# Kernel tuning notes

Measured on AMD Instinct MI355X. Metric: run time of the kernel, lower is better.

Reference implementation:

```python
import jax, jax.numpy as jnp
import numpy as np

NUM_CLASSES = 172
IGNORE_INDEX = 255
DICE_WEIGHT = 0.5
EPS = 1e-7


def setup_inputs() -> dict:
    key = jax.random.key(0)
    k1, k2 = jax.random.split(key)
    pred = jax.random.normal(k1, (4, NUM_CLASSES, 256, 256), dtype=jnp.float32)
    target = jax.random.randint(k2, (4, 256, 256), 0, NUM_CLASSES, dtype=jnp.int32)
    return {"pred": pred, "target": target}


def reference(pred, target):
    # pred: [B, C, H, W] logits; target: [B, H, W] int labels (255 = ignore)
    C = NUM_CLASSES
    logp = jax.nn.log_softmax(pred, axis=1)  # [B, C, H, W]

    # ---- cross entropy with ignore_index (mean over valid pixels) ----
    valid = target != IGNORE_INDEX  # [B, H, W]
    safe_tgt = jnp.where(valid, target, 0)
    nll = -jnp.take_along_axis(logp, safe_tgt[:, None].astype(jnp.int32), axis=1)[:, 0]  # [B, H, W]
    n_valid = jnp.sum(valid)
    ce = jnp.sum(jnp.where(valid, nll, 0.0)) / jnp.maximum(n_valid, 1).astype(pred.dtype)

    # ---- dice loss: vectorized over classes (replaces per-class python loop) ----
    p = jnp.exp(logp)  # softmax probs [B, C, H, W]
    # intersection[c] = sum over pixels with target==c of p[:, c] at those pixels
    gathered = jnp.take_along_axis(p, safe_tgt[:, None].astype(jnp.int32), axis=1)[:, 0]  # [B, H, W]
    seg_ids = target.ravel().astype(jnp.int32)  # ignore pixels land in bucket 255, discarded
    inter = jax.ops.segment_sum(gathered.ravel(), seg_ids, num_segments=256)[:C]  # [C]
    counts = jax.ops.segment_sum(jnp.ones_like(gathered.ravel()), seg_ids, num_segments=256)[:C]
    union = jnp.sum(p, axis=(0, 2, 3)) + counts  # [C]
    valid_c = union > 0
    dice_terms = jnp.where(valid_c, (2.0 * inter + EPS) / (union + EPS), 0.0)
    n_valid_c = jnp.sum(valid_c).astype(pred.dtype)
    dice = jnp.where(n_valid_c > 0, 1.0 - jnp.sum(dice_terms) / jnp.maximum(n_valid_c, 1.0), 0.0)

    return ce + DICE_WEIGHT * dice
```

## Files before the change

kernel.cpp:

```cpp
#include <hip/hip_runtime.h>
#include <stdint.h>

#define NCLS 172
#define IGN 255
#define HW 65536
#define NPIX 262144
#define EPSV 1e-7f
#define TP 128
#define NTHR 512
#define CPC 43
#define NSTAGE 32
#define SS 520

__global__ __launch_bounds__(NTHR) void seg_fused(
    const float* __restrict__ pred, const int* __restrict__ tgt,
    float* __restrict__ part)
{
    __shared__ float sPart[4 * TP];
    __shared__ float sInter[NCLS];
    __shared__ float sUnion[NCLS];
    __shared__ unsigned int sCnt[NCLS];
    __shared__ float sCE[2];

    const int tid   = threadIdx.x;
    const int lane  = tid & 63;
    const int p     = tid & (TP - 1);
    const int chunk = tid >> 7;
    const int c0    = chunk * CPC;

    for (int i = tid; i < NCLS; i += NTHR) { sInter[i] = 0.f; sUnion[i] = 0.f; sCnt[i] = 0u; }
    if (tid < 2) sCE[tid] = 0.f;

    const int pix0 = blockIdx.x * TP;
    const int b    = pix0 >> 16;
    const int hw0  = pix0 & (HW - 1);
    const float* gp = pred + (size_t)b * NCLS * HW + (size_t)c0 * HW + hw0 + p;

    float e[CPC];
    float s0 = 0.f, s1 = 0.f, s2 = 0.f, s3 = 0.f;
    #pragma unroll
    for (int k = 0; k < 40; k += 4) {
        e[k]     = __expf(gp[(size_t)(k    ) * HW]);
        e[k + 1] = __expf(gp[(size_t)(k + 1) * HW]);
        e[k + 2] = __expf(gp[(size_t)(k + 2) * HW]);
        e[k + 3] = __expf(gp[(size_t)(k + 3) * HW]);
        s0 += e[k]; s1 += e[k + 1]; s2 += e[k + 2]; s3 += e[k + 3];
    }
    e[40] = __expf(gp[(size_t)40 * HW]); s0 += e[40];
    e[41] = __expf(gp[(size_t)41 * HW]); s1 += e[41];
    e[42] = __expf(gp[(size_t)42 * HW]); s2 += e[42];
    sPart[chunk * TP + p] = (s0 + s1) + (s2 + s3);
    __syncthreads();

    const float s = (sPart[p] + sPart[TP + p]) + (sPart[2 * TP + p] + sPart[3 * TP + p]);
    const float invs = 1.0f / s;

    const int t = tgt[pix0 + p];
    const bool valid = (t != IGN);
    float nll = 0.f, nv = 0.f;
    if (valid && (t / CPC) == chunk) {
        const int kt = t - chunk * CPC;
        float et = 0.f;
        #pragma unroll
        for (int k = 0; k < CPC; ++k)
            if (kt == k) et = e[k];
        const float pt = et * invs;
        nll = -__logf(pt); nv = 1.f;
        atomicAdd(&sInter[t], pt);
        atomicAdd(&sCnt[t], 1u);
    }
    #pragma unroll
    for (int off = 32; off > 0; off >>= 1) {
        nll += __shfl_down(nll, off, 64);
        nv  += __shfl_down(nv,  off, 64);
    }
    if (lane == 0 && nv != 0.f) { atomicAdd(&sCE[0], nll); atomicAdd(&sCE[1], nv); }

    #pragma unroll
    for (int k = 0; k < CPC; ++k) {
        float v = e[k] * invs;
        #pragma unroll
        for (int m = 32; m > 0; m >>= 1) v += __shfl_xor(v, m, 64);
        if (lane == 0) atomicAdd(&sUnion[c0 + k], v);
    }
    __syncthreads();

    float* pb = part + (size_t)(blockIdx.x & (NSTAGE - 1)) * SS;
    if (tid < NCLS) {
        const float vi = sInter[tid];
        if (vi != 0.f) atomicAdd(&pb[tid], vi);
        const unsigned int ci = sCnt[tid];
        if (ci != 0u) atomicAdd(&pb[NCLS + tid], (float)ci);
        atomicAdd(&pb[344 + tid], sUnion[tid]);
    }
    if (tid == 0) { atomicAdd(&pb[516], sCE[0]); atomicAdd(&pb[517], sCE[1]); }
}

__global__ __launch_bounds__(256) void seg_fin(
    const float* __restrict__ part, float* __restrict__ out)
{
    __shared__ float sT[256], sN[256];
    const int tid = threadIdx.x;
    float term = 0.f, nv = 0.f;
    if (tid < NCLS) {
        float inter = 0.f, cnt = 0.f, uni = 0.f;
        for (int st = 0; st < NSTAGE; ++st) {
            inter += part[st * SS + tid];
            cnt   += part[st * SS + NCLS + tid];
            uni   += part[st * SS + 344 + tid];
        }
        const float u = uni + cnt;
        if (u > 0.f) { term = (2.f * inter + EPSV) / (u + EPSV); nv = 1.f; }
    }
    sT[tid] = term; sN[tid] = nv;
    __syncthreads();
    #pragma unroll
    for (int s2 = 128; s2 > 0; s2 >>= 1) {
        if (tid < s2) { sT[tid] += sT[tid + s2]; sN[tid] += sN[tid + s2]; }
        __syncthreads();
    }
    if (tid == 0) {
        float ce = 0.f, nvl = 0.f;
        for (int st = 0; st < NSTAGE; ++st) {
            ce  += part[st * SS + 516];
            nvl += part[st * SS + 517];
        }
        const float ceo  = ce / fmaxf(nvl, 1.f);
        const float dice = (sN[0] > 0.f) ? (1.f - sT[0] / fmaxf(sN[0], 1.f)) : 0.f;
        out[0] = ceo + 0.5f * dice;
    }
}

extern "C" void kernel_launch(void* const* d_in, const int* in_sizes, int n_in,
                              void* d_out, int out_size, void* d_ws, size_t ws_size,
                              hipStream_t stream) {
    const float* pred = (const float*)d_in[0];
    const int*   tgt  = (const int*)d_in[1];
    float* out  = (float*)d_out;
    float* part = (float*)d_ws;

    hipMemsetAsync(d_ws, 0, NSTAGE * SS * sizeof(float), stream);
    seg_fused<<<NPIX / TP, NTHR, 0, stream>>>(pred, tgt, part);
    seg_fin<<<1, 256, 0, stream>>>(part, out);
}
```

Measured before the change: 268.5 us.

## Split fused loss into sum-exp pass and per-class-group union pass with float4 loads

Replaces the single fused kernel, which held 43 exps per thread and did a wave shuffle-reduce per class, with two passes. The first pass atomically accumulates per-pixel sum-exp into a workspace buffer using float4 loads. The second pass re-reads the logits in blocks of 4 classes, normalises them with the stored sums, and accumulates union, intersection, count and NLL with far fewer reductions. The intent is to cut per-class shuffle and atomic overhead and register pressure, at the cost of reading pred twice and a larger memset.

```diff
diff --git a/kernel.cpp b/kernel.cpp
--- a/kernel.cpp
+++ b/kernel.cpp
@@ -6,94 +6,131 @@
 #define HW 65536
 #define NPIX 262144
 #define EPSV 1e-7f
-#define TP 128
-#define NTHR 512
-#define CPC 43
-#define NSTAGE 32
+#define NSTAGE 7
 #define SS 520
 
-__global__ __launch_bounds__(NTHR) void seg_fused(
-    const float* __restrict__ pred, const int* __restrict__ tgt,
-    float* __restrict__ part)
+__global__ __launch_bounds__(256) void seg_sumexp(
+    const float* __restrict__ pred, float* __restrict__ sum)
 {
-    __shared__ float sPart[4 * TP];
-    __shared__ float sInter[NCLS];
-    __shared__ float sUnion[NCLS];
-    __shared__ unsigned int sCnt[NCLS];
-    __shared__ float sCE[2];
+    const int bx = blockIdx.x;
+    const int sp = bx & 63;
+    const int cg = (bx >> 6) & 3;
+    const int b  = bx >> 8;
+    const int tid = threadIdx.x;
 
-    const int tid   = threadIdx.x;
-    const int lane  = tid & 63;
-    const int p     = tid & (TP - 1);
-    const int chunk = tid >> 7;
-    const int c0    = chunk * CPC;
+    const float4* gp = (const float4*)(pred
+        + (size_t)b * NCLS * HW + (size_t)(cg * 43) * HW + sp * 1024) + tid;
 
-    for (int i = tid; i < NCLS; i += NTHR) { sInter[i] = 0.f; sUnion[i] = 0.f; sCnt[i] = 0u; }
-    if (tid < 2) sCE[tid] = 0.f;
+    float s0 = 0.f, s1 = 0.f, s2 = 0.f, s3 = 0.f;
+    #pragma unroll 8
+    for (int k = 0; k < 43; ++k) {
+        const float4 x = gp[(size_t)k * (HW / 4)];
+        s0 += __expf(x.x); s1 += __expf(x.y);
+        s2 += __expf(x.z); s3 += __expf(x.w);
+    }
+    float* dp = sum + (size_t)b * HW + sp * 1024 + tid * 4;
+    atomicAdd(dp + 0, s0); atomicAdd(dp + 1, s1);
+    atomicAdd(dp + 2, s2); atomicAdd(dp + 3, s3);
+}
 
-    const int pix0 = blockIdx.x * TP;
-    const int b    = pix0 >> 16;
-    const int hw0  = pix0 & (HW - 1);
-    const float* gp = pred + (size_t)b * NCLS * HW + (size_t)c0 * HW + hw0 + p;
+__global__ __launch_bounds__(256) void seg_union(
+    const float* __restrict__ pred, const float* __restrict__ sum,
+    const int* __restrict__ tgt, float* __restrict__ part)
+{
+    const int bx = blockIdx.x;
+    const int sp = bx & 7;
+    const int b  = (bx >> 3) & 3;
+    const int cq = bx >> 5;
+    const int c0 = cq * 4;
+    const int tid = threadIdx.x, lane = tid & 63, wv = tid >> 6;
 
-    float e[CPC];
-    float s0 = 0.f, s1 = 0.f, s2 = 0.f, s3 = 0.f;
+    const size_t pixb = (size_t)b * HW + sp * 8192;
+    const float4* iv = (const float4*)(sum + pixb) + tid;
+    const int4*   tg = (const int4*)(tgt + pixb) + tid;
+    const float*  pb_base = pred + (size_t)b * NCLS * HW + sp * 8192;
+    const float4* p0 = (const float4*)(pb_base + (size_t)(c0 + 0) * HW) + tid;
+    const float4* p1 = (const float4*)(pb_base + (size_t)(c0 + 1) * HW) + tid;
+    const float4* p2 = (const float4*)(pb_base + (size_t)(c0 + 2) * HW) + tid;
+    const float4* p3 = (const float4*)(pb_base + (size_t)(c0 + 3) * HW) + tid;
+
+    float u0=0.f,u1=0.f,u2=0.f,u3=0.f;
+    float it0=0.f,it1=0.f,it2=0.f,it3=0.f;
+    float ct0=0.f,ct1=0.f,ct2=0.f,ct3=0.f;
+    float nll=0.f;
+
+    #pragma unroll 2
+    for (int j = 0; j < 8; ++j) {
+        const int idx = j * 256;
+        const float4 sv = iv[idx];
+        float4 inv;
+        inv.x = 1.f / sv.x; inv.y = 1.f / sv.y;
+        inv.z = 1.f / sv.z; inv.w = 1.f / sv.w;
+        const int4 t = tg[idx];
+
+        {   const float4 x = p0[idx];
+            const float ex=__expf(x.x), ey=__expf(x.y), ez=__expf(x.z), ew=__expf(x.w);
+            u0 += ex*inv.x + ey*inv.y + ez*inv.z + ew*inv.w;
+            if (t.x == c0) { const float pt=ex*inv.x; it0+=pt; ct0+=1.f; nll-=__logf(pt); }
+            if (t.y == c0) { const float pt=ey*inv.y; it0+=pt; ct0+=1.f; nll-=__logf(pt); }
+            if (t.z == c0) { const float pt=ez*inv.z; it0+=pt; ct0+=1.f; nll-=__logf(pt); }
+            if (t.w == c0) { const float pt=ew*inv.w; it0+=pt; ct0+=1.f; nll-=__logf(pt); }
+        }
+        {   const float4 x = p1[idx];
+            const float ex=__expf(x.x), ey=__expf(x.y), ez=__expf(x.z), ew=__expf(x.w);
+            u1 += ex*inv.x + ey*inv.y + ez*inv.z + ew*inv.w;
+            if (t.x == c0+1) { const float pt=ex*inv.x; it1+=pt; ct1+=1.f; nll-=__logf(pt); }
+            if (t.y == c0+1) { const float pt=ey*inv.y; it1+=pt; ct1+=1.f; nll-=__logf(pt); }
+            if (t.z == c0+1) { const float pt=ez*inv.z; it1+=pt; ct1+=1.f; nll-=__logf(pt); }
+            if (t.w == c0+1) { const float pt=ew*inv.w; it1+=pt; ct1+=1.f; nll-=__logf(pt); }
+        }
+        {   const float4 x = p2[idx];
+            const float ex=__expf(x.x), ey=__expf(x.y), ez=__expf(x.z), ew=__expf(x.w);
+            u2 += ex*inv.x + ey*inv.y + ez*inv.z + ew*inv.w;
+            if (t.x == c0+2) { const float pt=ex*inv.x; it2+=pt; ct2+=1.f; nll-=__logf(pt); }
+            if (t.y == c0+2) { const float pt=ey*inv.y; it2+=pt; ct2+=1.f; nll-=__logf(pt); }
+            if (t.z == c0+2) { const float pt=ez*inv.z; it2+=pt; ct2+=1.f; nll-=__logf(pt); }
+            if (t.w == c0+2) { const float pt=ew*inv.w; it2+=pt; ct2+=1.f; nll-=__logf(pt); }
+        }
+        {   const float4 x = p3[idx];
+            const float ex=__expf(x.x), ey=__expf(x.y), ez=__expf(x.z), ew=__expf(x.w);
+            u3 += ex*inv.x + ey*inv.y + ez*inv.z + ew*inv.w;
+            if (t.x == c0+3) { const float pt=ex*inv.x; it3+=pt; ct3+=1.f; nll-=__logf(pt); }
+            if (t.y == c0+3) { const float pt=ey*inv.y; it3+=pt; ct3+=1.f; nll-=__logf(pt); }
+            if (t.z == c0+3) { const float pt=ez*inv.z; it3+=pt; ct3+=1.f; nll-=__logf(pt); }
+            if (t.w == c0+3) { const float pt=ew*inv.w; it3+=pt; ct3+=1.f; nll-=__logf(pt); }
+        }
+    }
+
+    float vals[13] = {u0,u1,u2,u3, it0,it1,it2,it3, ct0,ct1,ct2,ct3, nll};
     #pragma unroll
-    for (int k = 0; k < 40; k += 4) {
-        e[k]     = __expf(gp[(size_t)(k    ) * HW]);
-        e[k + 1] = __expf(gp[(size_t)(k + 1) * HW]);
-        e[k + 2] = __expf(gp[(size_t)(k + 2) * HW]);
-        e[k + 3] = __expf(gp[(size_t)(k + 3) * HW]);
-        s0 += e[k]; s1 += e[k + 1]; s2 += e[k + 2]; s3 += e[k + 3];
-    }
-    e[40] = __expf(gp[(size_t)40 * HW]); s0 += e[40];
-    e[41] = __expf(gp[(size_t)41 * HW]); s1 += e[41];
-    e[42] = __expf(gp[(size_t)42 * HW]); s2 += e[42];
-    sPart[chunk * TP + p] = (s0 + s1) + (s2 + s3);
-    __syncthreads();
-
-    const float s = (sPart[p] + sPart[TP + p]) + (sPart[2 * TP + p] + sPart[3 * TP + p]);
-    const float invs = 1.0f / s;
-
-    const int t = tgt[pix0 + p];
-    const bool valid = (t != IGN);
-    float nll = 0.f, nv = 0.f;
-    if (valid && (t / CPC) == chunk) {
-        const int kt = t - chunk * CPC;
-        float et = 0.f;
-        #pragma unroll
-        for (int k = 0; k < CPC; ++k)
-            if (kt == k) et = e[k];
-        const float pt = et * invs;
-        nll = -__logf(pt); nv = 1.f;
-        atomicAdd(&sInter[t], pt);
-        atomicAdd(&sCnt[t], 1u);
-    }
-    #pragma unroll
-    for (int off = 32; off > 0; off >>= 1) {
-        nll += __shfl_down(nll, off, 64);
-        nv  += __shfl_down(nv,  off, 64);
-    }
-    if (lane == 0 && nv != 0.f) { atomicAdd(&sCE[0], nll); atomicAdd(&sCE[1], nv); }
-
-    #pragma unroll
-    for (int k = 0; k < CPC; ++k) {
-        float v = e[k] * invs;
+    for (int i = 0; i < 13; ++i) {
+        float v = vals[i];
         #pragma unroll
         for (int m = 32; m > 0; m >>= 1) v += __shfl_xor(v, m, 64);
-        if (lane == 0) atomicAdd(&sUnion[c0 + k], v);
+        vals[i] = v;
+    }
+    __shared__ float red[4][13];
+    if (lane == 0) {
+        #pragma unroll
+        for (int i = 0; i < 13; ++i) red[wv][i] = vals[i];
     }
     __syncthreads();
 
-    float* pb = part + (size_t)(blockIdx.x & (NSTAGE - 1)) * SS;
-    if (tid < NCLS) {
-        const float vi = sInter[tid];
-        if (vi != 0.f) atomicAdd(&pb[tid], vi);
-        const unsigned int ci = sCnt[tid];
-        if (ci != 0u) atomicAdd(&pb[NCLS + tid], (float)ci);
-        atomicAdd(&pb[344 + tid], sUnion[tid]);
+    float* pb = part + (size_t)(bx % NSTAGE) * SS;
+    if (tid < 13) {
+        const float v = red[0][tid] + red[1][tid] + red[2][tid] + red[3][tid];
+        if (tid < 4)       atomicAdd(&pb[344 + c0 + tid], v);
+        else if (tid < 8)  { if (v != 0.f) atomicAdd(&pb[c0 + tid - 4], v); }
+        else if (tid < 12) { if (v != 0.f) atomicAdd(&pb[172 + c0 + tid - 8], v); }
+        else               { if (v != 0.f) atomicAdd(&pb[516], v); }
     }
-    if (tid == 0) { atomicAdd(&pb[516], sCE[0]); atomicAdd(&pb[517], sCE[1]); }
+    if (tid == 13) {
+        float cs = 0.f;
+        #pragma unroll
+        for (int w = 0; w < 4; ++w)
+            cs += red[w][8] + red[w][9] + red[w][10] + red[w][11];
+        if (cs != 0.f) atomicAdd(&pb[517], cs);
+    }
 }
 
 __global__ __launch_bounds__(256) void seg_fin(
@@ -137,9 +174,13 @@
     const float* pred = (const float*)d_in[0];
     const int*   tgt  = (const int*)d_in[1];
     float* out  = (float*)d_out;
-    float* part = (float*)d_ws;
 
-    hipMemsetAsync(d_ws, 0, NSTAGE * SS * sizeof(float), stream);
-    seg_fused<<<NPIX / TP, NTHR, 0, stream>>>(pred, tgt, part);
+    char* ws = (char*)d_ws;
+    float* part = (float*)ws;
+    float* sum  = (float*)(ws + 16384);
+
+    hipMemsetAsync(d_ws, 0, 16384 + NPIX * 4, stream);
+    seg_sumexp<<<1024, 256, 0, stream>>>(pred, sum);
+    seg_union<<<1376, 256, 0, stream>>>(pred, sum, tgt, part);
     seg_fin<<<1, 256, 0, stream>>>(part, out);
 }
```

New measurement: 304.4 us. +13.4%, slower.
